# Performance work log

Hardware: AMD Instinct MI355X
Metric: run time of the kernel (lower is better)

## Reference

```python
import jax, jax.numpy as jnp
import numpy as np

C_IN = 64; C_OUT = 3; NG = 100; KS = 5; HID = 256; UR = 7; UC = 7
B = 4; H = 112; W = 112; SCALE = 2
Q = (H * SCALE) * (W * SCALE)

def _conv2d(x, w, b, pad):
    y = jax.lax.conv_general_dilated(x, w, (1, 1), ((pad, pad), (pad, pad)),
                                     dimension_numbers=('NCHW', 'OIHW', 'NCHW'))
    return y + b[None, :, None, None]

def _splat(feat, logits, sigma_x, sigma_y, opacity, rho, scale):
    # Gaussian splatting raster. H,W are multiples of (UR,UC) and scale is an int,
    # so the bicubic interpolations in the original are same-size identities.
    Bb, C, Hh, Ww = feat.shape
    nr, nc = Hh // UR, Ww // UC
    L = nr * nc; P = UR * UC
    uf = feat.reshape(Bb, C, nr, UR, nc, UC).transpose(0, 2, 4, 1, 3, 5).reshape(Bb * L, C, UR, UC)
    ul = logits.reshape(Bb, NG, nr, UR, nc, UC).transpose(0, 2, 4, 1, 3, 5).reshape(Bb * L, NG, UR, UC)
    sm = jax.nn.softmax(ul, axis=1)  # [BL,G,7,7]
    def wavg(v):
        return jnp.einsum('bgij,g->bij', sm, v).reshape(-1, P).mean(axis=0)  # [49]
    wsx, wsy, wop, wr = wavg(sigma_x), wavg(sigma_y), wavg(opacity), wavg(rho)
    c00 = wsx ** 2 + 1e-5; c11 = wsy ** 2 + 1e-5; c01 = wr * wsx * wsy
    det = c00 * c11 - c01 ** 2
    i00 = c11 / det; i11 = c00 / det; i01 = -c01 / det  # closed-form 2x2 inverse
    ax = jnp.linspace(-5.0, 5.0, KS)
    yy, xx = jnp.meshgrid(ax, ax, indexing='ij')
    z = -0.5 * (i00[:, None, None] * xx ** 2 + 2.0 * i01[:, None, None] * xx * yy
                + i11[:, None, None] * yy ** 2)
    kern = jnp.exp(z) / (2.0 * jnp.pi * jnp.sqrt(det))[:, None, None]
    kern = kern / kern.max(axis=(1, 2), keepdims=True)  # [49,5,5]
    kh = UR * scale; kw = UC * scale
    ph = kh - KS; pw = kw - KS
    kpad = jnp.pad(kern, ((0, 0), (ph // 2, ph - ph // 2), (pw // 2, pw - pw // 2)))
    # affine_grid translation + bilinear grid_sample (zeros padding, align_corners=True).
    # Kernels/translations are identical across batch and channel, so compute per-point only.
    pidx = jnp.arange(P)
    tx = (0.5 - (pidx // UC).astype(jnp.float32) / UR) * 2.0
    ty = (0.5 - (pidx % UC).astype(jnp.float32) / UC) * 2.0
    gx = jnp.linspace(-1.0, 1.0, kw)[None, None, :] + tx[:, None, None]
    gy = jnp.linspace(-1.0, 1.0, kh)[None, :, None] + ty[:, None, None]
    px = (gx + 1.0) * 0.5 * (kw - 1); py = (gy + 1.0) * 0.5 * (kh - 1)
    x0 = jnp.floor(px).astype(jnp.int32); y0 = jnp.floor(py).astype(jnp.int32)
    wx = px - x0; wy = py - y0
    def samp(yi, xi):
        v = kpad[pidx[:, None, None], jnp.clip(yi, 0, kh - 1), jnp.clip(xi, 0, kw - 1)]
        ok = (yi >= 0) & (yi < kh) & (xi >= 0) & (xi < kw)
        return jnp.where(ok, v, 0.0)
    kt = (samp(y0, x0) * (1 - wy) * (1 - wx) + samp(y0, x0 + 1) * (1 - wy) * wx
          + samp(y0 + 1, x0) * wy * (1 - wx) + samp(y0 + 1, x0 + 1) * wy * wx)  # [49,kh,kw]
    cols = uf.reshape(Bb * L, C, P).transpose(0, 2, 1) * wop[None, :, None]  # [BL,49,C]
    patches = jnp.clip(jnp.einsum('bpc,phw->bchw', cols, kt), 0.0, 1.0)  # splat + accumulate
    img = patches.reshape(Bb, nr, nc, C, kh, kw).transpose(0, 3, 1, 4, 2, 5)
    return img.reshape(Bb, C, nr * kh, nc * kw)

def _make_coord(h, w):
    ys = -1.0 + 1.0 / h + (2.0 / h) * jnp.arange(h, dtype=jnp.float32)
    xs = -1.0 + 1.0 / w + (2.0 / w) * jnp.arange(w, dtype=jnp.float32)
    return jnp.stack(jnp.meshgrid(ys, xs, indexing='ij'), axis=-1)  # [h,w,2] (y,x)

def _forward(feat, coord, cell, cls_w1, cls_b1, cls_w2, cls_b2, sigma_x, sigma_y,
             opacity, rho, coef_w, coef_b, freq_w, freq_b, phase_w,
             mlp_w1, mlp_b1, mlp_w2, mlp_b2, mlp_w3, mlp_b3, scale):
    h = jax.nn.relu(_conv2d(feat, cls_w1, cls_b1, 1))
    logits = _conv2d(h, cls_w2, cls_b2, 0)
    gfeat = _splat(feat, logits, sigma_x, sigma_y, opacity, rho, scale)  # [B,C,Ho,Wo]
    Bb = gfeat.shape[0]; Ho, Wo = gfeat.shape[2], gfeat.shape[3]
    coef = _conv2d(gfeat, coef_w, coef_b, 1)
    freq = _conv2d(gfeat, freq_w, freq_b, 1)
    # grid_sample nearest, align_corners=False (coord stored (y,x), flipped to (x,y))
    gx = coord[..., 1]; gy = coord[..., 0]
    ix = jnp.round(((gx + 1.0) * Wo - 1.0) * 0.5).astype(jnp.int32)
    iy = jnp.round(((gy + 1.0) * Ho - 1.0) * 0.5).astype(jnp.int32)
    ok = (ix >= 0) & (ix < Wo) & (iy >= 0) & (iy < Ho)
    ixc = jnp.clip(ix, 0, Wo - 1); iyc = jnp.clip(iy, 0, Ho - 1)
    bidx = jnp.arange(Bb)[:, None]
    q_coef = jnp.where(ok[..., None], coef[bidx, :, iyc, ixc], 0.0)  # [B,Q,HID]
    q_freq = jnp.where(ok[..., None], freq[bidx, :, iyc, ixc], 0.0)
    fc = _make_coord(Ho, Wo)
    q_coord = jnp.where(ok[..., None], fc[iyc, ixc], 0.0)  # [B,Q,2]
    sc = jnp.array([Ho, Wo], dtype=jnp.float32)
    rel_coord = (coord - q_coord) * sc
    rel_cell = cell * sc
    qf = q_freq.reshape(q_freq.shape[0], q_freq.shape[1], HID // 2, 2)
    s = jnp.einsum('bqki,bqi->bqk', qf, rel_coord) + rel_cell @ phase_w.T
    basis = jnp.concatenate([jnp.cos(jnp.pi * s), jnp.sin(jnp.pi * s)], axis=-1)
    x = q_coef * basis
    x = jax.nn.relu(x @ mlp_w1.T + mlp_b1)
    x = jax.nn.relu(x @ mlp_w2.T + mlp_b2)
    return x @ mlp_w3.T + mlp_b3  # [B,Q,3]

def setup_inputs():
    key = jax.random.key(0)
    ks = jax.random.split(key, 16)
    f32 = jnp.float32
    sx, sy = jnp.meshgrid(jnp.linspace(0.2, 3.0, 10), jnp.linspace(0.2, 3.0, 10), indexing='ij')
    return {
        'feat': jax.random.uniform(ks[0], (B, C_IN, H, W), f32),
        'coord': jax.random.uniform(ks[1], (B, Q, 2), f32, -1.0, 1.0),
        'cell': jnp.full((B, Q, 2), 2.0 / (H * SCALE), f32),
        'cls_w1': jax.random.normal(ks[2], (C_IN, C_IN, 3, 3), f32) * 0.02,
        'cls_b1': jnp.zeros((C_IN,), f32),
        'cls_w2': jax.random.normal(ks[3], (NG, C_IN, 1, 1), f32) * 0.02,
        'cls_b2': jnp.zeros((NG,), f32),
        'sigma_x': sx.reshape(-1).astype(f32),
        'sigma_y': sy.reshape(-1).astype(f32),
        'opacity': jax.random.uniform(ks[4], (NG,), f32, 0.3, 0.9),
        'rho': jax.random.uniform(ks[5], (NG,), f32, -0.5, 0.5),
        'coef_w': jax.random.normal(ks[6], (HID, C_IN, 3, 3), f32) * 0.02,
        'coef_b': jnp.zeros((HID,), f32),
        'freq_w': jax.random.normal(ks[7], (HID, C_IN, 3, 3), f32) * 0.02,
        'freq_b': jnp.zeros((HID,), f32),
        'phase_w': jax.random.normal(ks[8], (HID // 2, 2), f32) * 0.5,
        'mlp_w1': jax.random.normal(ks[9], (HID, HID), f32) * 0.05,
        'mlp_b1': jnp.zeros((HID,), f32),
        'mlp_w2': jax.random.normal(ks[10], (HID, HID), f32) * 0.05,
        'mlp_b2': jnp.zeros((HID,), f32),
        'mlp_w3': jax.random.normal(ks[11], (C_OUT, HID), f32) * 0.05,
        'mlp_b3': jnp.zeros((C_OUT,), f32),
        'scale': SCALE,
    }

def reference(feat, coord, cell, cls_w1, cls_b1, cls_w2, cls_b2, sigma_x, sigma_y,
              opacity, rho, coef_w, coef_b, freq_w, freq_b, phase_w,
              mlp_w1, mlp_b1, mlp_w2, mlp_b2, mlp_w3, mlp_b3, scale):
    return _forward(feat, coord, cell, cls_w1, cls_b1, cls_w2, cls_b2, sigma_x, sigma_y,
                    opacity, rho, coef_w, coef_b, freq_w, freq_b, phase_w,
                    mlp_w1, mlp_b1, mlp_w2, mlp_b2, mlp_w3, mlp_b3, scale)
```

## Files before the change

kernel.cpp:

```cpp
#include <hip/hip_runtime.h>
#include <hip/hip_fp16.h>
#include <math.h>

namespace {
constexpr int kB   = 4;
constexpr int kNG  = 100;
constexpr int kH1  = 112;
constexpr int kH2  = 224;
constexpr int kQ   = kH2 * kH2;
constexpr int kP1  = kH1 * kH1;

constexpr size_t B_FBH  = 0;
constexpr size_t B_FBL  = 6422528;
constexpr size_t B_GFH  = 0;
constexpr size_t B_GFL  = 6422528;
constexpr size_t B_H    = 12845056;
constexpr size_t B_CF   = 25690112;
constexpr size_t B_WBASE= B_CF + 51380224;

constexpr size_t A_FBH  = 0;
constexpr size_t A_FBL  = 6422528;
constexpr size_t A_H    = 12845056;
constexpr size_t A_GFH  = 0;
constexpr size_t A_GFL  = 25690112;
constexpr size_t A_CF   = 51380224;
constexpr size_t A_WBASE= A_CF + 205520896;
constexpr size_t A_TOTAL= A_WBASE + 1893376;

constexpr size_t W_WPH  = 0;
constexpr size_t W_WPL  = 589824;
constexpr size_t W_W1H  = 1179648;
constexpr size_t W_W1L  = 1253376;
constexpr size_t W_WMLP = 1327104;
constexpr size_t W_WSUM = 1851392;
constexpr size_t W_WK   = 1852416;
}

using s8v = __attribute__((ext_vector_type(8))) short;
using f4v = __attribute__((ext_vector_type(4))) float;
using u4v = __attribute__((ext_vector_type(4))) unsigned int;

__device__ __forceinline__ unsigned short f2bf(float f) {
  unsigned int u = __float_as_uint(f);
  unsigned int r = u + 0x7fffu + ((u >> 16) & 1u);
  return (unsigned short)(r >> 16);
}
__device__ __forceinline__ float bf2f(unsigned short h) {
  return __uint_as_float((unsigned int)h << 16);
}
__device__ __forceinline__ unsigned short f2h(float f) {
  return __builtin_bit_cast(unsigned short, __float2half(f));
}
__device__ __forceinline__ float h2f(unsigned short u) {
  return __half2float(__builtin_bit_cast(__half, u));
}

__global__ void k_init(float* wsums) {
  int t = threadIdx.x;
  if (t < 196) wsums[t] = 0.0f;
}

__global__ __launch_bounds__(256) void k_prepfeat(const float* __restrict__ feat,
                                                  unsigned short* __restrict__ fbh,
                                                  unsigned short* __restrict__ fbl) {
  __shared__ float ls[64 * 65];
  const int t = threadIdx.x;
  const int b = blockIdx.x / 196;
  const int seg = blockIdx.x % 196;
  const int pixbase = seg * 64;
  for (int idx = t; idx < 4096; idx += 256) {
    int ci = idx >> 6, px = idx & 63;
    ls[px * 65 + ci] = feat[((size_t)(b * 64 + ci)) * kP1 + pixbase + px];
  }
  __syncthreads();
  for (int idx = t; idx < 4096; idx += 256) {
    int px = idx >> 6, ci = idx & 63;
    float v = ls[px * 65 + ci];
    unsigned short hi = f2bf(v);
    unsigned short lo = f2bf(v - bf2f(hi));
    size_t o = ((size_t)(b * kP1 + pixbase + px)) * 64 + ci;
    fbh[o] = hi;
    fbl[o] = lo;
  }
}

__global__ void k_prepw(const float* __restrict__ cw, const float* __restrict__ fw,
                        unsigned short* __restrict__ wph, unsigned short* __restrict__ wpl) {
  int e = blockIdx.x * 256 + threadIdx.x;
  int co = e / 576, k = e % 576;
  int ci = k & 63, kk = k >> 6;
  float v = (co < 256) ? cw[co * 576 + ci * 9 + kk] : fw[(co - 256) * 576 + ci * 9 + kk];
  unsigned short hi = f2bf(v);
  unsigned short lo = f2bf(v - bf2f(hi));
  int n16 = co >> 4, nl = co & 15;
  int kstep = k >> 5, kr = k & 31;
  int dst = ((n16 * 18 + kstep) * 64 + (kr >> 3) * 16 + nl) * 8 + (kr & 7);
  wph[dst] = hi;
  wpl[dst] = lo;
}

__global__ void k_prepw1(const float* __restrict__ w1src,
                         unsigned short* __restrict__ wph, unsigned short* __restrict__ wpl) {
  int e = blockIdx.x * 256 + threadIdx.x;
  int co = e / 576, k = e % 576;
  int ci = k & 63, kk = k >> 6;
  float v = w1src[co * 576 + ci * 9 + kk];
  unsigned short hi = f2bf(v);
  unsigned short lo = f2bf(v - bf2f(hi));
  int n16 = co >> 4, nl = co & 15;
  int kstep = k >> 5, kr = k & 31;
  int dst = ((n16 * 18 + kstep) * 64 + (kr >> 3) * 16 + nl) * 8 + (kr & 7);
  wph[dst] = hi;
  wpl[dst] = lo;
}

__global__ void k_prepmlp(const float* __restrict__ w1, const float* __restrict__ w2,
                          unsigned short* __restrict__ wp) {
  int e = blockIdx.x * 256 + threadIdx.x;
  int mat = e >> 16, idx = e & 65535;
  int j = idx >> 8, k = idx & 255;
  float v = (mat ? w2 : w1)[j * 256 + k];
  unsigned short hi = f2bf(v);
  unsigned short lo = f2bf(v - bf2f(hi));
  int n16 = j >> 4, nl = j & 15;
  int kstep = k >> 5, kr = k & 31;
  int dst = ((n16 * 8 + kstep) * 64 + (kr >> 3) * 16 + nl) * 8 + (kr & 7);
  wp[mat * 131072 + dst] = hi;
  wp[mat * 131072 + 65536 + dst] = lo;
}

__global__ __launch_bounds__(256) void k_conv1_mfma(
    const unsigned short* __restrict__ fbh, const unsigned short* __restrict__ fbl,
    const unsigned short* __restrict__ wph, const unsigned short* __restrict__ wpl,
    const float* __restrict__ bias, float* __restrict__ outp) {
  __shared__ __attribute__((aligned(16))) char Asb[2 * 180 * 144];
  const int t = threadIdx.x;
  const int blk = blockIdx.x;
  const int b = blk / 98;
  const int mt = blk % 98;
  const int ty = mt / 14, tx = mt % 14;
  const int py0 = ty * 16, px0 = tx * 8;

  for (int idx = t; idx < 2880; idx += 256) {
    int plane = idx >= 1440;
    int r2 = plane ? idx - 1440 : idx;
    int p = r2 >> 3, c8 = r2 & 7;
    int pr = p / 10, pc = p % 10;
    int gy = py0 - 1 + pr, gx = px0 - 1 + pc;
    uint4 u = make_uint4(0u, 0u, 0u, 0u);
    if (gy >= 0 && gy < kH1 && gx >= 0 && gx < kH1) {
      const unsigned short* src = (plane ? fbl : fbh) +
          ((size_t)(b * kP1 + gy * kH1 + gx)) * 64 + c8 * 8;
      u = *(const uint4*)src;
    }
    *(uint4*)(Asb + plane * 25920 + p * 144 + c8 * 16) = u;
  }
  __syncthreads();

  const int w = t >> 6, lane = t & 63;
  const int quad = lane >> 4, ml = lane & 15;

  f4v acc[8];
#pragma unroll
  for (int i = 0; i < 8; ++i) acc[i] = (f4v){0.0f, 0.0f, 0.0f, 0.0f};

  const unsigned int bvoff = (unsigned int)lane * 16u;
#pragma unroll
  for (int kk = 0; kk < 9; ++kk) {
    const int ky = kk / 3, kx = kk % 3;
#pragma unroll
    for (int cs = 0; cs < 2; ++cs) {
      const int kstep = kk * 2 + cs;
      unsigned int off = ((unsigned int)(w * 18 + kstep)) * 1024u + bvoff;
      s8v Bh = *(const s8v*)((const char*)wph + off);
      s8v Bl = *(const s8v*)((const char*)wpl + off);
#pragma unroll
      for (int i = 0; i < 8; ++i) {
        const int aoff = ((2 * i + (ml >> 3) + ky) * 10 + (ml & 7) + kx) * 144 + cs * 64 + quad * 16;
        s8v Ah = *(const s8v*)(Asb + aoff);
        s8v Al = *(const s8v*)(Asb + 25920 + aoff);
        acc[i] = __builtin_amdgcn_mfma_f32_16x16x32_bf16(Ah, Bh, acc[i], 0, 0, 0);
        acc[i] = __builtin_amdgcn_mfma_f32_16x16x32_bf16(Al, Bh, acc[i], 0, 0, 0);
        acc[i] = __builtin_amdgcn_mfma_f32_16x16x32_bf16(Ah, Bl, acc[i], 0, 0, 0);
      }
    }
  }

  const float bv = bias[w * 16 + ml];
#pragma unroll
  for (int i = 0; i < 8; ++i)
#pragma unroll
    for (int reg = 0; reg < 4; ++reg) {
      int m = i * 16 + quad * 4 + reg;
      int Y = py0 + (m >> 3), X = px0 + (m & 7);
      outp[((size_t)(b * kP1 + Y * kH1 + X)) * 64 + w * 16 + ml] =
          fmaxf(acc[i][reg] + bv, 0.0f);
    }
}

__global__ __launch_bounds__(256) void k_wavg(
    const float* __restrict__ h, const float* __restrict__ w2, const float* __restrict__ b2,
    const float* __restrict__ sx, const float* __restrict__ sy,
    const float* __restrict__ op, const float* __restrict__ rho,
    float* __restrict__ wsums) {
  __shared__ float w2s[kNG * 64];
  __shared__ float prm[4 * kNG];
  __shared__ float b2s[kNG];
  __shared__ float pl[196];
  const int t = threadIdx.x;
  for (int i = t; i < kNG * 64; i += 256) w2s[i] = w2[i];
  if (t < kNG) {
    prm[t] = sx[t];
    prm[kNG + t] = sy[t];
    prm[2 * kNG + t] = op[t];
    prm[3 * kNG + t] = rho[t];
    b2s[t] = b2[t];
  }
  if (t < 196) pl[t] = 0.0f;
  __syncthreads();
  const int id = blockIdx.x * 256 + t;
  float hreg[64];
  const float4* hp = (const float4*)(h + (size_t)id * 64);
#pragma unroll
  for (int i = 0; i < 16; ++i) {
    float4 v = hp[i];
    hreg[4 * i] = v.x; hreg[4 * i + 1] = v.y;
    hreg[4 * i + 2] = v.z; hreg[4 * i + 3] = v.w;
  }
  float S = 0, Sx = 0, Sy = 0, So = 0, Sr = 0;
  for (int g = 0; g < kNG; ++g) {
    float d = b2s[g];
    const float4* wp = (const float4*)(w2s + g * 64);
#pragma unroll
    for (int i = 0; i < 16; ++i) {
      float4 w = wp[i];
      d += hreg[4 * i] * w.x + hreg[4 * i + 1] * w.y +
           hreg[4 * i + 2] * w.z + hreg[4 * i + 3] * w.w;
    }
    float e = expf(d);
    S += e;
    Sx += e * prm[g];
    Sy += e * prm[kNG + g];
    So += e * prm[2 * kNG + g];
    Sr += e * prm[3 * kNG + g];
  }
  const int rem = id % (kH1 * kH1);
  const int p = ((rem / kH1) % 7) * 7 + ((rem % kH1) % 7);
  const float inv = 1.0f / S;
  atomicAdd(&pl[p], Sx * inv);
  atomicAdd(&pl[49 + p], Sy * inv);
  atomicAdd(&pl[98 + p], So * inv);
  atomicAdd(&pl[147 + p], Sr * inv);
  __syncthreads();
  if (t < 196) atomicAdd(&wsums[t], pl[t]);
}

__global__ __launch_bounds__(256) void k_finalize(const float* __restrict__ wsums,
                                                  float* __restrict__ wk) {
  __shared__ float kern_s[49 * 25];
  __shared__ float wavg_s[196];
  const int t = threadIdx.x;
  if (t < 196) wavg_s[t] = wsums[t] * (1.0f / 1024.0f);
  __syncthreads();
  if (t < 49) {
    float wsx = wavg_s[t], wsy = wavg_s[49 + t], wr = wavg_s[147 + t];
    float c00 = wsx * wsx + 1e-5f;
    float c11 = wsy * wsy + 1e-5f;
    float c01 = wr * wsx * wsy;
    float det = c00 * c11 - c01 * c01;
    float i00 = c11 / det, i11 = c00 / det, i01 = -c01 / det;
    float nrm = 1.0f / (2.0f * 3.14159265358979323846f * sqrtf(det));
    float vals[25];
    float mx = -1e30f;
#pragma unroll
    for (int i = 0; i < 5; ++i) {
#pragma unroll
      for (int j = 0; j < 5; ++j) {
        float yv = -5.0f + 2.5f * (float)i;
        float xv = -5.0f + 2.5f * (float)j;
        float z = -0.5f * (i00 * xv * xv + 2.0f * i01 * xv * yv + i11 * yv * yv);
        float v = expf(z) * nrm;
        vals[i * 5 + j] = v;
        mx = fmaxf(mx, v);
      }
    }
#pragma unroll
    for (int k = 0; k < 25; ++k) kern_s[t * 25 + k] = vals[k] / mx;
  }
  __syncthreads();
  for (int idx = t; idx < 49 * 196; idx += 256) {
    const int p = idx / 196;
    const int hw = idx % 196;
    const int hh = hw / 14, ww = hw % 14;
    float txv = (0.5f - (float)(p / 7) / 7.0f) * 2.0f;
    float tyv = (0.5f - (float)(p % 7) / 7.0f) * 2.0f;
    float gxv = (-1.0f + (float)ww * (2.0f / 13.0f)) + txv;
    float gyv = (-1.0f + (float)hh * (2.0f / 13.0f)) + tyv;
    float pxv = (gxv + 1.0f) * 0.5f * 13.0f;
    float pyv = (gyv + 1.0f) * 0.5f * 13.0f;
    float x0f = floorf(pxv), y0f = floorf(pyv);
    int x0 = (int)x0f, y0 = (int)y0f;
    float wx = pxv - x0f, wy = pyv - y0f;
    auto samp = [&](int yi, int xi) -> float {
      if (yi < 4 || yi >= 9 || xi < 4 || xi >= 9) return 0.0f;
      return kern_s[p * 25 + (yi - 4) * 5 + (xi - 4)];
    };
    float kt = samp(y0, x0) * (1.0f - wy) * (1.0f - wx) +
               samp(y0, x0 + 1) * (1.0f - wy) * wx +
               samp(y0 + 1, x0) * wy * (1.0f - wx) +
               samp(y0 + 1, x0 + 1) * wy * wx;
    wk[idx] = wavg_s[98 + p] * kt;
  }
}

__global__ __launch_bounds__(256) void k_splat(const float* __restrict__ feat,
                                               const float* __restrict__ wk,
                                               unsigned short* __restrict__ gfh,
                                               unsigned short* __restrict__ gfl) {
  __shared__ float fs[64 * 49];
  __shared__ float wks[49 * 196];
  const int t = threadIdx.x;
  const int b = blockIdx.x >> 8;
  const int rem = blockIdx.x & 255;
  const int ry = rem >> 4, rx = rem & 15;
  const float* featb = feat + (size_t)b * 64 * kP1;
  for (int idx = t; idx < 64 * 49; idx += 256) {
    int ci = idx / 49, p = idx % 49;
    int gy = ry * 7 + p / 7, gx = rx * 7 + p % 7;
    fs[idx] = featb[((size_t)ci * kH1 + gy) * kH1 + gx];
  }
  for (int idx = t; idx < 49 * 196; idx += 256) wks[idx] = wk[idx];
  __syncthreads();
  const int ci = t & 63;
  const int s = t >> 6;
  const int h0 = (s >> 1) * 7, w0 = (s & 1) * 7;
  float acc[49];
#pragma unroll
  for (int i = 0; i < 49; ++i) acc[i] = 0.0f;
  for (int p = 0; p < 49; ++p) {
    float f = fs[ci * 49 + p];
#pragma unroll
    for (int i = 0; i < 7; ++i)
#pragma unroll
      for (int j = 0; j < 7; ++j)
        acc[i * 7 + j] += f * wks[p * 196 + (h0 + i) * 14 + (w0 + j)];
  }
#pragma unroll
  for (int i = 0; i < 7; ++i)
#pragma unroll
    for (int j = 0; j < 7; ++j) {
      int Y = ry * 14 + h0 + i;
      int X = rx * 14 + w0 + j;
      float v = fminf(fmaxf(acc[i * 7 + j], 0.0f), 1.0f);
      unsigned short hi = f2bf(v);
      unsigned short lo = f2bf(v - bf2f(hi));
      size_t o = ((size_t)(b * kQ + Y * kH2 + X)) * 64 + ci;
      gfh[o] = hi;
      gfl[o] = lo;
    }
}

__global__ __launch_bounds__(256) void k_conv2_mfma(
    const unsigned short* __restrict__ gfh, const unsigned short* __restrict__ gfl,
    const unsigned short* __restrict__ wph, const unsigned short* __restrict__ wpl,
    const float* __restrict__ coef_b, const float* __restrict__ freq_b,
    unsigned short* __restrict__ outp) {
  __shared__ __attribute__((aligned(16))) char Asb[2 * 180 * 144];
  const int t = threadIdx.x;
  const int b = blockIdx.x / 784;
  const int blk = blockIdx.x % 784;
  const int nb = blk & 1;
  const int mt = blk >> 1;
  const int ty = mt / 28, tx = mt % 28;
  const int py0 = ty * 16, px0 = tx * 8;

  for (int idx = t; idx < 2880; idx += 256) {
    int plane = idx >= 1440;
    int r2 = plane ? idx - 1440 : idx;
    int p = r2 >> 3, c8 = r2 & 7;
    int pr = p / 10, pc = p % 10;
    int gy = py0 - 1 + pr, gx = px0 - 1 + pc;
    uint4 u = make_uint4(0u, 0u, 0u, 0u);
    if (gy >= 0 && gy < kH2 && gx >= 0 && gx < kH2) {
      const unsigned short* src = (plane ? gfl : gfh) +
          ((size_t)(b * kQ + gy * kH2 + gx)) * 64 + c8 * 8;
      u = *(const uint4*)src;
    }
    *(uint4*)(Asb + plane * 25920 + p * 144 + c8 * 16) = u;
  }
  __syncthreads();

  const int w = t >> 6, lane = t & 63;
  const int quad = lane >> 4, ml = lane & 15;
  const int abase = (((ml >> 3) * 10) + (ml & 7)) * 144 + quad * 16;
  const int n16base = nb * 16 + w * 4;
  const unsigned int bvoff = (unsigned int)lane * 16u;

  f4v acc[8][4];
#pragma unroll
  for (int i = 0; i < 8; ++i)
#pragma unroll
    for (int j = 0; j < 4; ++j) acc[i][j] = (f4v){0.0f, 0.0f, 0.0f, 0.0f};

#pragma unroll
  for (int kk = 0; kk < 9; ++kk) {
    const int ky = kk / 3, kx = kk % 3;
#pragma unroll
    for (int cs = 0; cs < 2; ++cs) {
      const int kstep = kk * 2 + cs;
      s8v Bh[4], Bl[4];
#pragma unroll
      for (int j = 0; j < 4; ++j) {
        unsigned int off = ((unsigned int)(n16base + j) * 18u + (unsigned int)kstep) * 1024u + bvoff;
        Bh[j] = *(const s8v*)((const char*)wph + off);
        Bl[j] = *(const s8v*)((const char*)wpl + off);
      }
#pragma unroll
      for (int i = 0; i < 8; ++i) {
        const int aoff = ((2 * i + ky) * 10 + kx) * 144 + cs * 64 + abase;
        s8v Ah = *(const s8v*)(Asb + aoff);
        s8v Al = *(const s8v*)(Asb + 25920 + aoff);
#pragma unroll
        for (int j = 0; j < 4; ++j) {
          acc[i][j] = __builtin_amdgcn_mfma_f32_16x16x32_bf16(Ah, Bh[j], acc[i][j], 0, 0, 0);
          acc[i][j] = __builtin_amdgcn_mfma_f32_16x16x32_bf16(Al, Bh[j], acc[i][j], 0, 0, 0);
          acc[i][j] = __builtin_amdgcn_mfma_f32_16x16x32_bf16(Ah, Bl[j], acc[i][j], 0, 0, 0);
        }
      }
    }
  }

  const int cobase = nb * 256 + w * 64;
  float bj[4];
#pragma unroll
  for (int j = 0; j < 4; ++j) {
    int co = cobase + j * 16 + ml;
    bj[j] = (co < 256) ? coef_b[co] : freq_b[co - 256];
  }
  __syncthreads();
  float* Ls = (float*)Asb;
  const int pq = t >> 3;
  const int ts = t & 7;
#pragma unroll
  for (int c = 0; c < 4; ++c) {
#pragma unroll
    for (int ii = 0; ii < 2; ++ii) {
      const int i = c * 2 + ii;
#pragma unroll
      for (int j = 0; j < 4; ++j)
#pragma unroll
        for (int reg = 0; reg < 4; ++reg) {
          const int p = ii * 16 + quad * 4 + reg;
          Ls[p * 268 + w * 64 + j * 16 + ml] = acc[i][j][reg] + bj[j];
        }
    }
    __syncthreads();
    const int m = c * 32 + pq;
    const int Y = py0 + (m >> 3), X = px0 + (m & 7);
    unsigned short* orow = outp + ((size_t)(b * kQ + Y * kH2 + X)) * 512 + nb * 256;
    const float* lrow = Ls + pq * 268;
#pragma unroll
    for (int u = 0; u < 4; ++u) {
      float4 a = *(const float4*)(lrow + u * 64 + ts * 8);
      float4 bb = *(const float4*)(lrow + u * 64 + ts * 8 + 4);
      u4v v;
      v.x = (unsigned)f2h(a.x) | ((unsigned)f2h(a.y) << 16);
      v.y = (unsigned)f2h(a.z) | ((unsigned)f2h(a.w) << 16);
      v.z = (unsigned)f2h(bb.x) | ((unsigned)f2h(bb.y) << 16);
      v.w = (unsigned)f2h(bb.z) | ((unsigned)f2h(bb.w) << 16);
      __builtin_nontemporal_store(v, (u4v*)(orow + u * 64 + ts * 8));
    }
    __syncthreads();
  }
}

__global__ __launch_bounds__(256) void k_query_mfma(
    const unsigned short* __restrict__ cfh,
    const float* __restrict__ coord,
    const float* __restrict__ cell, const float* __restrict__ phw,
    const unsigned short* __restrict__ wmlp,
    const float* __restrict__ b1, const float* __restrict__ b2,
    const float* __restrict__ w3, const float* __restrict__ b3,
    float* __restrict__ out, int q_base, size_t cf_stride) {
  __shared__ __attribute__((aligned(16))) char Xs[2 * 32 * 264 * 2];
  constexpr int ROW = 264 * 2;
  constexpr int PLANE = 32 * 264 * 2;
  const int t = threadIdx.x;

  {
    const int tq = t >> 3, ts = t & 7;
    const int qg = q_base + blockIdx.x * 32 + tq;
    const int b = qg / kQ;
    float gy = coord[(size_t)qg * 2 + 0];
    float gx = coord[(size_t)qg * 2 + 1];
    float fx = ((gx + 1.0f) * 224.0f - 1.0f) * 0.5f;
    float fy = ((gy + 1.0f) * 224.0f - 1.0f) * 0.5f;
    int ix = (int)rintf(fx);
    int iy = (int)rintf(fy);
    bool ok = (ix >= 0) && (ix < 224) && (iy >= 0) && (iy < 224);
    int ixc = min(max(ix, 0), 223);
    int iyc = min(max(iy, 0), 223);
    float m = ok ? 1.0f : 0.0f;
    float qcy = ok ? (-1.0f + (1.0f / 224.0f) + (2.0f / 224.0f) * (float)iyc) : 0.0f;
    float qcx = ok ? (-1.0f + (1.0f / 224.0f) + (2.0f / 224.0f) * (float)ixc) : 0.0f;
    float rel0 = (gy - qcy) * 224.0f;
    float rel1 = (gx - qcx) * 224.0f;
    float rc0 = cell[(size_t)qg * 2 + 0] * 224.0f;
    float rc1 = cell[(size_t)qg * 2 + 1] * 224.0f;
    const unsigned short* base = cfh + (size_t)b * cf_stride +
                                 (((size_t)iyc * kH2 + ixc) * 512);
    unsigned short ch_[8], cl_[8], sh_[8], sl_[8];
#pragma unroll
    for (int u = 0; u < 4; ++u) {
      const int k4 = ts * 16 + u * 4;
      ushort4 clo = *(const ushort4*)(base + k4);
      ushort4 chi = *(const ushort4*)(base + 128 + k4);
      ushort4 f0 = *(const ushort4*)(base + 256 + 2 * k4);
      ushort4 f1 = *(const ushort4*)(base + 256 + 2 * k4 + 4);
      float fr[8] = {h2f(f0.x), h2f(f0.y), h2f(f0.z), h2f(f0.w),
                     h2f(f1.x), h2f(f1.y), h2f(f1.z), h2f(f1.w)};
      float cl4[4] = {h2f(clo.x), h2f(clo.y), h2f(clo.z), h2f(clo.w)};
      float ch4[4] = {h2f(chi.x), h2f(chi.y), h2f(chi.z), h2f(chi.w)};
#pragma unroll
      for (int e = 0; e < 4; ++e) {
        const int k = k4 + e;
        float ph = rc0 * phw[2 * k] + rc1 * phw[2 * k + 1];
        float s = m * (fr[2 * e] * rel0 + fr[2 * e + 1] * rel1) + ph;
        float sv, cv;
        sincospif(s, &sv, &cv);
        float xc = m * cl4[e] * cv;
        float xsn = m * ch4[e] * sv;
        const int sl = (u & 1) * 4 + e;
        unsigned short h1_ = f2bf(xc);
        ch_[sl] = h1_; cl_[sl] = f2bf(xc - bf2f(h1_));
        unsigned short h2_ = f2bf(xsn);
        sh_[sl] = h2_; sl_[sl] = f2bf(xsn - bf2f(h2_));
      }
      if (u & 1) {
        const int kb = ts * 16 + (u - 1) * 4;
        uint4 v;
        v.x = (unsigned)ch_[0] | ((unsigned)ch_[1] << 16);
        v.y = (unsigned)ch_[2] | ((unsigned)ch_[3] << 16);
        v.z = (unsigned)ch_[4] | ((unsigned)ch_[5] << 16);
        v.w = (unsigned)ch_[6] | ((unsigned)ch_[7] << 16);
        *(uint4*)(Xs + tq * ROW + kb * 2) = v;
        v.x = (unsigned)cl_[0] | ((unsigned)cl_[1] << 16);
        v.y = (unsigned)cl_[2] | ((unsigned)cl_[3] << 16);
        v.z = (unsigned)cl_[4] | ((unsigned)cl_[5] << 16);
        v.w = (unsigned)cl_[6] | ((unsigned)cl_[7] << 16);
        *(uint4*)(Xs + PLANE + tq * ROW + kb * 2) = v;
        v.x = (unsigned)sh_[0] | ((unsigned)sh_[1] << 16);
        v.y = (unsigned)sh_[2] | ((unsigned)sh_[3] << 16);
        v.z = (unsigned)sh_[4] | ((unsigned)sh_[5] << 16);
        v.w = (unsigned)sh_[6] | ((unsigned)sh_[7] << 16);
        *(uint4*)(Xs + tq * ROW + (128 + kb) * 2) = v;
        v.x = (unsigned)sl_[0] | ((unsigned)sl_[1] << 16);
        v.y = (unsigned)sl_[2] | ((unsigned)sl_[3] << 16);
        v.z = (unsigned)sl_[4] | ((unsigned)sl_[5] << 16);
        v.w = (unsigned)sl_[6] | ((unsigned)sl_[7] << 16);
        *(uint4*)(Xs + PLANE + tq * ROW + (128 + kb) * 2) = v;
      }
    }
  }
  __syncthreads();

  const int w = t >> 6, lane = t & 63;
  const int quad = lane >> 4, ml = lane & 15;
  const unsigned int bvoff = (unsigned int)lane * 16u;

#pragma unroll
  for (int layer = 0; layer < 2; ++layer) {
    const unsigned short* wb = wmlp + layer * 131072;
    f4v acc[2][4];
#pragma unroll
    for (int i = 0; i < 2; ++i)
#pragma unroll
      for (int j = 0; j < 4; ++j) acc[i][j] = (f4v){0.0f, 0.0f, 0.0f, 0.0f};
#pragma unroll
    for (int kstep = 0; kstep < 8; ++kstep) {
      s8v Bh[4], Bl[4];
#pragma unroll
      for (int j = 0; j < 4; ++j) {
        unsigned int off = (unsigned int)((w * 4 + j) * 8 + kstep) * 1024u + bvoff;
        Bh[j] = *(const s8v*)((const char*)wb + off);
        Bl[j] = *(const s8v*)((const char*)(wb + 65536) + off);
      }
#pragma unroll
      for (int i = 0; i < 2; ++i) {
        const int aoff = (i * 16 + ml) * ROW + (kstep * 32 + quad * 8) * 2;
        s8v Ah = *(const s8v*)(Xs + aoff);
        s8v Al = *(const s8v*)(Xs + PLANE + aoff);
#pragma unroll
        for (int j = 0; j < 4; ++j) {
          acc[i][j] = __builtin_amdgcn_mfma_f32_16x16x32_bf16(Ah, Bh[j], acc[i][j], 0, 0, 0);
          acc[i][j] = __builtin_amdgcn_mfma_f32_16x16x32_bf16(Al, Bh[j], acc[i][j], 0, 0, 0);
          acc[i][j] = __builtin_amdgcn_mfma_f32_16x16x32_bf16(Ah, Bl[j], acc[i][j], 0, 0, 0);
        }
      }
    }
    __syncthreads();
    const float* bs = layer ? b2 : b1;
    float bj[4];
#pragma unroll
    for (int j = 0; j < 4; ++j) bj[j] = bs[w * 64 + j * 16 + ml];
    if (layer == 0) {
#pragma unroll
      for (int i = 0; i < 2; ++i)
#pragma unroll
        for (int j = 0; j < 4; ++j)
#pragma unroll
          for (int reg = 0; reg < 4; ++reg) {
            int m = i * 16 + quad * 4 + reg;
            int n = w * 64 + j * 16 + ml;
            float v = fmaxf(acc[i][j][reg] + bj[j], 0.0f);
            unsigned short hi = f2bf(v);
            unsigned short lo = f2bf(v - bf2f(hi));
            *(unsigned short*)(Xs + m * ROW + n * 2) = hi;
            *(unsigned short*)(Xs + PLANE + m * ROW + n * 2) = lo;
          }
    } else {
#pragma unroll
      for (int i = 0; i < 2; ++i)
#pragma unroll
        for (int j = 0; j < 4; ++j)
#pragma unroll
          for (int reg = 0; reg < 4; ++reg) {
            int m = i * 16 + quad * 4 + reg;
            int n = w * 64 + j * 16 + ml;
            float v = fmaxf(acc[i][j][reg] + bj[j], 0.0f);
            *(float*)(Xs + ((size_t)m * 264 + n) * 4) = v;
          }
    }
    __syncthreads();
  }

  {
    const int tq = t >> 3, ts = t & 7;
    const float* xr = (const float*)(Xs + (size_t)tq * 264 * 4);
    float c0 = 0, c1 = 0, c2 = 0;
    for (int k = ts * 32; k < ts * 32 + 32; ++k) {
      float xv = xr[k];
      c0 += xv * w3[k];
      c1 += xv * w3[256 + k];
      c2 += xv * w3[512 + k];
    }
    c0 += __shfl_down(c0, 4, 8); c0 += __shfl_down(c0, 2, 8); c0 += __shfl_down(c0, 1, 8);
    c1 += __shfl_down(c1, 4, 8); c1 += __shfl_down(c1, 2, 8); c1 += __shfl_down(c1, 1, 8);
    c2 += __shfl_down(c2, 4, 8); c2 += __shfl_down(c2, 2, 8); c2 += __shfl_down(c2, 1, 8);
    if (ts == 0) {
      const int qg = q_base + blockIdx.x * 32 + tq;
      float* o = out + (size_t)qg * 3;
      o[0] = c0 + b3[0];
      o[1] = c1 + b3[1];
      o[2] = c2 + b3[2];
    }
  }
}

extern "C" void kernel_launch(void* const* d_in, const int* in_sizes, int n_in,
                              void* d_out, int out_size, void* d_ws, size_t ws_size,
                              hipStream_t stream) {
  (void)in_sizes; (void)n_in; (void)out_size;
  const float* feat   = (const float*)d_in[0];
  const float* coord  = (const float*)d_in[1];
  const float* cell   = (const float*)d_in[2];
  const float* cls_w1 = (const float*)d_in[3];
  const float* cls_b1 = (const float*)d_in[4];
  const float* cls_w2 = (const float*)d_in[5];
  const float* cls_b2 = (const float*)d_in[6];
  const float* sigx   = (const float*)d_in[7];
  const float* sigy   = (const float*)d_in[8];
  const float* opac   = (const float*)d_in[9];
  const float* rho    = (const float*)d_in[10];
  const float* coef_w = (const float*)d_in[11];
  const float* coef_b = (const float*)d_in[12];
  const float* freq_w = (const float*)d_in[13];
  const float* freq_b = (const float*)d_in[14];
  const float* phw    = (const float*)d_in[15];
  const float* w1     = (const float*)d_in[16];
  const float* b1     = (const float*)d_in[17];
  const float* w2     = (const float*)d_in[18];
  const float* b2     = (const float*)d_in[19];
  const float* w3     = (const float*)d_in[20];
  const float* b3     = (const float*)d_in[21];

  const bool big = ws_size >= A_TOTAL;
  char* ws = (char*)d_ws;
  const size_t wbase = big ? A_WBASE : B_WBASE;
  unsigned short* fbh = (unsigned short*)(ws + (big ? A_FBH : B_FBH));
  unsigned short* fbl = (unsigned short*)(ws + (big ? A_FBL : B_FBL));
  unsigned short* gfh = (unsigned short*)(ws + (big ? A_GFH : B_GFH));
  unsigned short* gfl = (unsigned short*)(ws + (big ? A_GFL : B_GFL));
  float* h_buf = (float*)(ws + (big ? A_H : B_H));
  unsigned short* cfb = (unsigned short*)(ws + (big ? A_CF : B_CF));
  unsigned short* wph = (unsigned short*)(ws + wbase + W_WPH);
  unsigned short* wpl = (unsigned short*)(ws + wbase + W_WPL);
  unsigned short* w1h = (unsigned short*)(ws + wbase + W_W1H);
  unsigned short* w1l = (unsigned short*)(ws + wbase + W_W1L);
  unsigned short* wmlp = (unsigned short*)(ws + wbase + W_WMLP);
  float* wsums = (float*)(ws + wbase + W_WSUM);
  float* wk    = (float*)(ws + wbase + W_WK);
  float* outp  = (float*)d_out;

  hipLaunchKernelGGL(k_init, dim3(1), dim3(256), 0, stream, wsums);
  hipLaunchKernelGGL(k_prepw, dim3(1152), dim3(256), 0, stream, coef_w, freq_w, wph, wpl);
  hipLaunchKernelGGL(k_prepw1, dim3(144), dim3(256), 0, stream, cls_w1, w1h, w1l);
  hipLaunchKernelGGL(k_prepmlp, dim3(512), dim3(256), 0, stream, w1, w2, wmlp);
  hipLaunchKernelGGL(k_prepfeat, dim3(784), dim3(256), 0, stream, feat, fbh, fbl);
  hipLaunchKernelGGL(k_conv1_mfma, dim3(392), dim3(256), 0, stream,
                     fbh, fbl, w1h, w1l, cls_b1, h_buf);
  hipLaunchKernelGGL(k_wavg, dim3(196), dim3(256), 0, stream,
                     h_buf, cls_w2, cls_b2, sigx, sigy, opac, rho, wsums);
  hipLaunchKernelGGL(k_finalize, dim3(1), dim3(256), 0, stream, wsums, wk);

  if (big) {
    hipLaunchKernelGGL(k_splat, dim3(4 * 256), dim3(256), 0, stream, feat, wk, gfh, gfl);
    hipLaunchKernelGGL(k_conv2_mfma, dim3(4 * 784), dim3(256), 0, stream,
                       gfh, gfl, wph, wpl, coef_b, freq_b, cfb);
    hipLaunchKernelGGL(k_query_mfma, dim3(4 * 1568), dim3(256), 0, stream,
                       cfb, coord, cell, phw, wmlp, b1, b2, w3, b3, outp,
                       0, (size_t)kQ * 512);
  } else {
    for (int b = 0; b < kB; ++b) {
      const float* feat_b = feat + (size_t)b * 64 * kP1;
      hipLaunchKernelGGL(k_splat, dim3(256), dim3(256), 0, stream, feat_b, wk, gfh, gfl);
      hipLaunchKernelGGL(k_conv2_mfma, dim3(784), dim3(256), 0, stream,
                         gfh, gfl, wph, wpl, coef_b, freq_b, cfb);
      hipLaunchKernelGGL(k_query_mfma, dim3(1568), dim3(256), 0, stream,
                         cfb, coord, cell, phw, wmlp, b1, b2, w3, b3, outp,
                         b * kQ, (size_t)0);
    }
  }
}
```

Before: 884.9 us.

## Split MFMA warp tiles 2x2 across M and N in conv and MLP kernels

Changes the per-wave work split in the conv GEMM and the query MLP GEMM. Each wave now covers half of the M rows and half of the N columns (a 4x8 or 1x8 tile) instead of all M rows and a quarter of N. Each wave loads more B fragments per k-step and fewer A fragments. That shifts pressure from LDS A reads to global or L2 weight reads and raises the register count for B. The conv epilogue is restructured to write 16 rows per pass over 8 passes, which doubles the number of barrier rounds.

After: 903.6 us. 2.1% more time.

```diff
diff --git a/kernel.cpp b/kernel.cpp
--- a/kernel.cpp
+++ b/kernel.cpp
@@ -392,15 +392,15 @@
 
   const int w = t >> 6, lane = t & 63;
   const int quad = lane >> 4, ml = lane & 15;
-  const int abase = (((ml >> 3) * 10) + (ml & 7)) * 144 + quad * 16;
-  const int n16base = nb * 16 + w * 4;
+  const int mh = w & 1;
+  const int nh = w >> 1;
   const unsigned int bvoff = (unsigned int)lane * 16u;
 
-  f4v acc[8][4];
-#pragma unroll
-  for (int i = 0; i < 8; ++i)
-#pragma unroll
-    for (int j = 0; j < 4; ++j) acc[i][j] = (f4v){0.0f, 0.0f, 0.0f, 0.0f};
+  f4v acc[4][8];
+#pragma unroll
+  for (int i = 0; i < 4; ++i)
+#pragma unroll
+    for (int j = 0; j < 8; ++j) acc[i][j] = (f4v){0.0f, 0.0f, 0.0f, 0.0f};
 
 #pragma unroll
   for (int kk = 0; kk < 9; ++kk) {
@@ -408,20 +408,21 @@
 #pragma unroll
     for (int cs = 0; cs < 2; ++cs) {
       const int kstep = kk * 2 + cs;
-      s8v Bh[4], Bl[4];
-#pragma unroll
-      for (int j = 0; j < 4; ++j) {
-        unsigned int off = ((unsigned int)(n16base + j) * 18u + (unsigned int)kstep) * 1024u + bvoff;
+      s8v Bh[8], Bl[8];
+#pragma unroll
+      for (int j = 0; j < 8; ++j) {
+        unsigned int off = ((unsigned int)((nb * 16 + nh * 8 + j) * 18 + kstep)) * 1024u + bvoff;
         Bh[j] = *(const s8v*)((const char*)wph + off);
         Bl[j] = *(const s8v*)((const char*)wpl + off);
       }
 #pragma unroll
-      for (int i = 0; i < 8; ++i) {
-        const int aoff = ((2 * i + ky) * 10 + kx) * 144 + cs * 64 + abase;
+      for (int i = 0; i < 4; ++i) {
+        const int aoff = ((mh * 8 + 2 * i + (ml >> 3) + ky) * 10 + (ml & 7) + kx) * 144 +
+                         cs * 64 + quad * 16;
         s8v Ah = *(const s8v*)(Asb + aoff);
         s8v Al = *(const s8v*)(Asb + 25920 + aoff);
 #pragma unroll
-        for (int j = 0; j < 4; ++j) {
+        for (int j = 0; j < 8; ++j) {
           acc[i][j] = __builtin_amdgcn_mfma_f32_16x16x32_bf16(Ah, Bh[j], acc[i][j], 0, 0, 0);
           acc[i][j] = __builtin_amdgcn_mfma_f32_16x16x32_bf16(Al, Bh[j], acc[i][j], 0, 0, 0);
           acc[i][j] = __builtin_amdgcn_mfma_f32_16x16x32_bf16(Ah, Bl[j], acc[i][j], 0, 0, 0);
@@ -430,45 +431,41 @@
     }
   }
 
-  const int cobase = nb * 256 + w * 64;
-  float bj[4];
-#pragma unroll
-  for (int j = 0; j < 4; ++j) {
-    int co = cobase + j * 16 + ml;
+  float bj[8];
+#pragma unroll
+  for (int j = 0; j < 8; ++j) {
+    int co = nb * 256 + nh * 128 + j * 16 + ml;
     bj[j] = (co < 256) ? coef_b[co] : freq_b[co - 256];
   }
   __syncthreads();
   float* Ls = (float*)Asb;
-  const int pq = t >> 3;
-  const int ts = t & 7;
-#pragma unroll
-  for (int c = 0; c < 4; ++c) {
-#pragma unroll
-    for (int ii = 0; ii < 2; ++ii) {
-      const int i = c * 2 + ii;
-#pragma unroll
-      for (int j = 0; j < 4; ++j)
-#pragma unroll
-        for (int reg = 0; reg < 4; ++reg) {
-          const int p = ii * 16 + quad * 4 + reg;
-          Ls[p * 268 + w * 64 + j * 16 + ml] = acc[i][j][reg] + bj[j];
-        }
+  const int pq = t >> 4;
+  const int ts2 = t & 15;
+#pragma unroll
+  for (int c = 0; c < 8; ++c) {
+    if ((c >> 2) == mh) {
+      const int i = c & 3;
+#pragma unroll
+      for (int j = 0; j < 8; ++j)
+#pragma unroll
+        for (int reg = 0; reg < 4; ++reg)
+          Ls[(quad * 4 + reg) * 268 + nh * 128 + j * 16 + ml] = acc[i][j][reg] + bj[j];
     }
     __syncthreads();
-    const int m = c * 32 + pq;
+    const int m = c * 16 + pq;
     const int Y = py0 + (m >> 3), X = px0 + (m & 7);
     unsigned short* orow = outp + ((size_t)(b * kQ + Y * kH2 + X)) * 512 + nb * 256;
     const float* lrow = Ls + pq * 268;
 #pragma unroll
-    for (int u = 0; u < 4; ++u) {
-      float4 a = *(const float4*)(lrow + u * 64 + ts * 8);
-      float4 bb = *(const float4*)(lrow + u * 64 + ts * 8 + 4);
+    for (int u = 0; u < 2; ++u) {
+      float4 a = *(const float4*)(lrow + ts2 * 16 + u * 8);
+      float4 bb = *(const float4*)(lrow + ts2 * 16 + u * 8 + 4);
       u4v v;
       v.x = (unsigned)f2h(a.x) | ((unsigned)f2h(a.y) << 16);
       v.y = (unsigned)f2h(a.z) | ((unsigned)f2h(a.w) << 16);
       v.z = (unsigned)f2h(bb.x) | ((unsigned)f2h(bb.y) << 16);
       v.w = (unsigned)f2h(bb.z) | ((unsigned)f2h(bb.w) << 16);
-      __builtin_nontemporal_store(v, (u4v*)(orow + u * 64 + ts * 8));
+      __builtin_nontemporal_store(v, (u4v*)(orow + ts2 * 16 + u * 8));
     }
     __syncthreads();
   }
@@ -566,70 +563,63 @@
 
   const int w = t >> 6, lane = t & 63;
   const int quad = lane >> 4, ml = lane & 15;
+  const int mh = w & 1;
+  const int nh = w >> 1;
   const unsigned int bvoff = (unsigned int)lane * 16u;
 
 #pragma unroll
   for (int layer = 0; layer < 2; ++layer) {
     const unsigned short* wb = wmlp + layer * 131072;
-    f4v acc[2][4];
-#pragma unroll
-    for (int i = 0; i < 2; ++i)
-#pragma unroll
-      for (int j = 0; j < 4; ++j) acc[i][j] = (f4v){0.0f, 0.0f, 0.0f, 0.0f};
+    f4v acc[8];
+#pragma unroll
+    for (int j = 0; j < 8; ++j) acc[j] = (f4v){0.0f, 0.0f, 0.0f, 0.0f};
 #pragma unroll
     for (int kstep = 0; kstep < 8; ++kstep) {
-      s8v Bh[4], Bl[4];
-#pragma unroll
-      for (int j = 0; j < 4; ++j) {
-        unsigned int off = (unsigned int)((w * 4 + j) * 8 + kstep) * 1024u + bvoff;
+      s8v Bh[8], Bl[8];
+#pragma unroll
+      for (int j = 0; j < 8; ++j) {
+        unsigned int off = (unsigned int)((nh * 8 + j) * 8 + kstep) * 1024u + bvoff;
         Bh[j] = *(const s8v*)((const char*)wb + off);
         Bl[j] = *(const s8v*)((const char*)(wb + 65536) + off);
       }
-#pragma unroll
-      for (int i = 0; i < 2; ++i) {
-        const int aoff = (i * 16 + ml) * ROW + (kstep * 32 + quad * 8) * 2;
-        s8v Ah = *(const s8v*)(Xs + aoff);
-        s8v Al = *(const s8v*)(Xs + PLANE + aoff);
-#pragma unroll
-        for (int j = 0; j < 4; ++j) {
-          acc[i][j] = __builtin_amdgcn_mfma_f32_16x16x32_bf16(Ah, Bh[j], acc[i][j], 0, 0, 0);
-          acc[i][j] = __builtin_amdgcn_mfma_f32_16x16x32_bf16(Al, Bh[j], acc[i][j], 0, 0, 0);
-          acc[i][j] = __builtin_amdgcn_mfma_f32_16x16x32_bf16(Ah, Bl[j], acc[i][j], 0, 0, 0);
-        }
+      const int aoff = (mh * 16 + ml) * ROW + (kstep * 32 + quad * 8) * 2;
+      s8v Ah = *(const s8v*)(Xs + aoff);
+      s8v Al = *(const s8v*)(Xs + PLANE + aoff);
+#pragma unroll
+      for (int j = 0; j < 8; ++j) {
+        acc[j] = __builtin_amdgcn_mfma_f32_16x16x32_bf16(Ah, Bh[j], acc[j], 0, 0, 0);
+        acc[j] = __builtin_amdgcn_mfma_f32_16x16x32_bf16(Al, Bh[j], acc[j], 0, 0, 0);
+        acc[j] = __builtin_amdgcn_mfma_f32_16x16x32_bf16(Ah, Bl[j], acc[j], 0, 0, 0);
       }
     }
     __syncthreads();
     const float* bs = layer ? b2 : b1;
-    float bj[4];
-#pragma unroll
-    for (int j = 0; j < 4; ++j) bj[j] = bs[w * 64 + j * 16 + ml];
+    float bj[8];
+#pragma unroll
+    for (int j = 0; j < 8; ++j) bj[j] = bs[nh * 128 + j * 16 + ml];
     if (layer == 0) {
 #pragma unroll
-      for (int i = 0; i < 2; ++i)
-#pragma unroll
-        for (int j = 0; j < 4; ++j)
-#pragma unroll
-          for (int reg = 0; reg < 4; ++reg) {
-            int m = i * 16 + quad * 4 + reg;
-            int n = w * 64 + j * 16 + ml;
-            float v = fmaxf(acc[i][j][reg] + bj[j], 0.0f);
-            unsigned short hi = f2bf(v);
-            unsigned short lo = f2bf(v - bf2f(hi));
-            *(unsigned short*)(Xs + m * ROW + n * 2) = hi;
-            *(unsigned short*)(Xs + PLANE + m * ROW + n * 2) = lo;
-          }
+      for (int j = 0; j < 8; ++j)
+#pragma unroll
+        for (int reg = 0; reg < 4; ++reg) {
+          int m = mh * 16 + quad * 4 + reg;
+          int n = nh * 128 + j * 16 + ml;
+          float v = fmaxf(acc[j][reg] + bj[j], 0.0f);
+          unsigned short hi = f2bf(v);
+          unsigned short lo = f2bf(v - bf2f(hi));
+          *(unsigned short*)(Xs + m * ROW + n * 2) = hi;
+          *(unsigned short*)(Xs + PLANE + m * ROW + n * 2) = lo;
+        }
     } else {
 #pragma unroll
-      for (int i = 0; i < 2; ++i)
-#pragma unroll
-        for (int j = 0; j < 4; ++j)
-#pragma unroll
-          for (int reg = 0; reg < 4; ++reg) {
-            int m = i * 16 + quad * 4 + reg;
-            int n = w * 64 + j * 16 + ml;
-            float v = fmaxf(acc[i][j][reg] + bj[j], 0.0f);
-            *(float*)(Xs + ((size_t)m * 264 + n) * 4) = v;
-          }
+      for (int j = 0; j < 8; ++j)
+#pragma unroll
+        for (int reg = 0; reg < 4; ++reg) {
+          int m = mh * 16 + quad * 4 + reg;
+          int n = nh * 128 + j * 16 + ml;
+          float v = fmaxf(acc[j][reg] + bj[j], 0.0f);
+          *(float*)(Xs + ((size_t)m * 264 + n) * 4) = v;
+        }
     }
     __syncthreads();
   }
```
